# Performance work log

Hardware: AMD Instinct MI355X
Metric: run time of the kernel (lower is better)

The kernel has to match this reference:

```python
import jax, jax.numpy as jnp
import numpy as np


def setup_inputs() -> dict:
    key = jax.random.key(0)
    k1, k2 = jax.random.split(key)
    x1 = jax.random.normal(k1, (2048, 64), dtype=jnp.float32)
    x2 = jax.random.normal(k2, (2048, 64), dtype=jnp.float32)
    return {"x1": x1, "x2": x2}


def reference(x1, x2):
    # Faithful to L1Distance._dist with postprocess=identity (gpytorch default),
    # x1_eq_x2=False.
    adjustment = jnp.mean(x1, axis=-2, keepdims=True)  # [1, D]
    x1c = x1 - adjustment
    x2c = x2 - adjustment
    # pairwise L1: [N1, N2, D] broadcast, abs, sum over D -> [N1, N2]
    res = jnp.sum(jnp.abs(x1c[:, None, :] - x2c[None, :, :]), axis=-1)
    res = jnp.maximum(res, 0.0)  # clamp_min_(0)
    return res
```

## Files before the change

kernel.cpp:

```cpp
#include <hip/hip_runtime.h>


#define TILE 64
#define PAD  68
#define D_FIXED 64

__global__ __launch_bounds__(256, 4)
void l1dist_kernel(const float* __restrict__ x1, const float* __restrict__ x2,
                   float* __restrict__ out, int N1, int N2) {
    __shared__ float s1[TILE * PAD];
    __shared__ float s2[TILE * PAD];

    const int bi = blockIdx.y;
    const int bj = blockIdx.x;
    const int tx = threadIdx.x;
    const int ty = threadIdx.y;
    const int t  = ty * 16 + tx;

    const float* g1 = x1 + (size_t)bi * TILE * D_FIXED;
    const float* g2 = x2 + (size_t)bj * TILE * D_FIXED;
    #pragma unroll
    for (int f = 0; f < 4; ++f) {
        int idx = t + f * 256;
        int row = idx >> 4;
        int c4  = (idx & 15) << 2;
        float4 v1 = *(const float4*)(g1 + row * D_FIXED + c4);
        float4 v2 = *(const float4*)(g2 + row * D_FIXED + c4);
        *(float4*)(s1 + row * PAD + c4) = v1;
        *(float4*)(s2 + row * PAD + c4) = v2;
    }
    __syncthreads();

    float acc[4][4];
    #pragma unroll
    for (int i = 0; i < 4; ++i)
        #pragma unroll
        for (int j = 0; j < 4; ++j) acc[i][j] = 0.0f;

    #pragma unroll
    for (int d = 0; d < D_FIXED; d += 4) {
        float4 a[4], b[4];
        #pragma unroll
        for (int r = 0; r < 4; ++r)
            a[r] = *(const float4*)(s1 + (ty + 16 * r) * PAD + d);
        #pragma unroll
        for (int r = 0; r < 4; ++r)
            b[r] = *(const float4*)(s2 + (tx + 16 * r) * PAD + d);

        #pragma unroll
        for (int i = 0; i < 4; ++i) {
            #pragma unroll
            for (int j = 0; j < 4; ++j) {
                float d0 = a[i].x - b[j].x;
                float d1 = a[i].y - b[j].y;
                float d2 = a[i].z - b[j].z;
                float d3 = a[i].w - b[j].w;
                acc[i][j] += (fabsf(d0) + fabsf(d1)) + (fabsf(d2) + fabsf(d3));
            }
        }
    }

    const int i0 = bi * TILE;
    const int j0 = bj * TILE;
    #pragma unroll
    for (int ri = 0; ri < 4; ++ri) {
        int i = i0 + ty + 16 * ri;
        #pragma unroll
        for (int rj = 0; rj < 4; ++rj) {
            int j = j0 + tx + 16 * rj;
            out[(size_t)i * N2 + j] = acc[ri][rj];
        }
    }
}

extern "C" void kernel_launch(void* const* d_in, const int* in_sizes, int n_in,
                              void* d_out, int out_size, void* d_ws, size_t ws_size,
                              hipStream_t stream) {
    const float* x1 = (const float*)d_in[0];
    const float* x2 = (const float*)d_in[1];
    float* out = (float*)d_out;

    const int N1 = in_sizes[0] / D_FIXED;
    const int N2 = in_sizes[1] / D_FIXED;

    dim3 block(16, 16);
    dim3 grid(N2 / TILE, N1 / TILE);
    l1dist_kernel<<<grid, block, 0, stream>>>(x1, x2, out, N1, N2);
}
```

Before: 70.41 us.

## Replace shared-memory tiled L1 kernel with register-resident x2 row per thread

Each thread now holds one full 64-float row of x2 in registers and loops over 16 rows of x1, reading them straight from global memory as wavefront-uniform broadcast loads. Shared memory staging and the block barrier are gone, and output stores become coalesced across j. In exchange each thread carries a large register footprint, which may limit occupancy, and every x1 row is reloaded from global/L2 by each block, losing the 4x4 register-tile reuse the old version had.

```diff
diff --git a/kernel.cpp b/kernel.cpp
--- a/kernel.cpp
+++ b/kernel.cpp
@@ -1,75 +1,37 @@
 #include <hip/hip_runtime.h>
 
 
-#define TILE 64
-#define PAD  68
 #define D_FIXED 64
+#define ROWS 16
 
 __global__ __launch_bounds__(256, 4)
 void l1dist_kernel(const float* __restrict__ x1, const float* __restrict__ x2,
                    float* __restrict__ out, int N1, int N2) {
-    __shared__ float s1[TILE * PAD];
-    __shared__ float s2[TILE * PAD];
+    const int j  = blockIdx.x * 256 + threadIdx.x;
+    const int i0 = blockIdx.y * ROWS;
 
-    const int bi = blockIdx.y;
-    const int bj = blockIdx.x;
-    const int tx = threadIdx.x;
-    const int ty = threadIdx.y;
-    const int t  = ty * 16 + tx;
-
-    const float* g1 = x1 + (size_t)bi * TILE * D_FIXED;
-    const float* g2 = x2 + (size_t)bj * TILE * D_FIXED;
-    #pragma unroll
-    for (int f = 0; f < 4; ++f) {
-        int idx = t + f * 256;
-        int row = idx >> 4;
-        int c4  = (idx & 15) << 2;
-        float4 v1 = *(const float4*)(g1 + row * D_FIXED + c4);
-        float4 v2 = *(const float4*)(g2 + row * D_FIXED + c4);
-        *(float4*)(s1 + row * PAD + c4) = v1;
-        *(float4*)(s2 + row * PAD + c4) = v2;
-    }
-    __syncthreads();
-
-    float acc[4][4];
-    #pragma unroll
-    for (int i = 0; i < 4; ++i)
-        #pragma unroll
-        for (int j = 0; j < 4; ++j) acc[i][j] = 0.0f;
-
+    float v[D_FIXED];
+    const float* p2 = x2 + (size_t)j * D_FIXED;
     #pragma unroll
     for (int d = 0; d < D_FIXED; d += 4) {
-        float4 a[4], b[4];
-        #pragma unroll
-        for (int r = 0; r < 4; ++r)
-            a[r] = *(const float4*)(s1 + (ty + 16 * r) * PAD + d);
-        #pragma unroll
-        for (int r = 0; r < 4; ++r)
-            b[r] = *(const float4*)(s2 + (tx + 16 * r) * PAD + d);
-
-        #pragma unroll
-        for (int i = 0; i < 4; ++i) {
-            #pragma unroll
-            for (int j = 0; j < 4; ++j) {
-                float d0 = a[i].x - b[j].x;
-                float d1 = a[i].y - b[j].y;
-                float d2 = a[i].z - b[j].z;
-                float d3 = a[i].w - b[j].w;
-                acc[i][j] += (fabsf(d0) + fabsf(d1)) + (fabsf(d2) + fabsf(d3));
-            }
-        }
+        float4 q = *(const float4*)(p2 + d);
+        v[d + 0] = q.x; v[d + 1] = q.y; v[d + 2] = q.z; v[d + 3] = q.w;
     }
 
-    const int i0 = bi * TILE;
-    const int j0 = bj * TILE;
-    #pragma unroll
-    for (int ri = 0; ri < 4; ++ri) {
-        int i = i0 + ty + 16 * ri;
+    #pragma unroll 2
+    for (int r = 0; r < ROWS; ++r) {
+        const int i = i0 + r;
+        const float* p1 = x1 + (size_t)i * D_FIXED;
+        float a0 = 0.f, a1 = 0.f, a2 = 0.f, a3 = 0.f;
         #pragma unroll
-        for (int rj = 0; rj < 4; ++rj) {
-            int j = j0 + tx + 16 * rj;
-            out[(size_t)i * N2 + j] = acc[ri][rj];
+        for (int d = 0; d < D_FIXED; d += 4) {
+            float4 q = *(const float4*)(p1 + d);
+            a0 += fabsf(q.x - v[d + 0]);
+            a1 += fabsf(q.y - v[d + 1]);
+            a2 += fabsf(q.z - v[d + 2]);
+            a3 += fabsf(q.w - v[d + 3]);
         }
+        out[(size_t)i * N2 + j] = (a0 + a1) + (a2 + a3);
     }
 }
 
@@ -83,7 +45,7 @@
     const int N1 = in_sizes[0] / D_FIXED;
     const int N2 = in_sizes[1] / D_FIXED;
 
-    dim3 block(16, 16);
-    dim3 grid(N2 / TILE, N1 / TILE);
+    dim3 block(256);
+    dim3 grid(N2 / 256, N1 / ROWS);
     l1dist_kernel<<<grid, block, 0, stream>>>(x1, x2, out, N1, N2);
 }
```

Result: slower. 89.35 us (+26.9%).
